# Performance work log

Hardware: AMD Instinct MI355X
Metric: run time of the kernel (lower is better)

Reference implementation:

```python
import jax, jax.numpy as jnp
import numpy as np

L, D, F, H = 4, 1024, 2048, 8
DH = D // H
EPS = 1e-5


def setup_inputs() -> dict:
    key = jax.random.key(0)
    ks = jax.random.split(key, 8)
    B, S = 4, 1024
    sd = 1.0 / np.sqrt(D)
    sf = 1.0 / np.sqrt(F)
    return {
        "X": jax.random.normal(ks[0], (B, S, D), jnp.float32),
        "Wq": jax.random.normal(ks[1], (L, D, D), jnp.float32) * sd,
        "Wk": jax.random.normal(ks[2], (L, D, D), jnp.float32) * sd,
        "Wv": jax.random.normal(ks[3], (L, D, D), jnp.float32) * sd,
        "Wg": jax.random.normal(ks[4], (L, D, D), jnp.float32) * sd,
        "Wo": jax.random.normal(ks[5], (L, D, D), jnp.float32) * sd,
        "W1": jax.random.normal(ks[6], (L, D, F), jnp.float32) * sd,
        "W2": jax.random.normal(ks[7], (L, F, D), jnp.float32) * sf,
        "ln_scale": jnp.ones((D,), jnp.float32),
        "ln_bias": jnp.zeros((D,), jnp.float32),
        "gn_scale": jnp.ones((L, D), jnp.float32),
        "gn_bias": jnp.zeros((L, D), jnp.float32),
    }


def _layer_norm(x, scale, bias):
    mu = x.mean(-1, keepdims=True)
    var = x.var(-1, keepdims=True)
    return (x - mu) * jax.lax.rsqrt(var + EPS) * scale + bias


def _rotate(x, cos, sin):
    # x: (B,S,H,DH); cos/sin: (1,S,1,DH//2); rotary pairs (even, odd)
    x1, x2 = x[..., 0::2], x[..., 1::2]
    r1 = x1 * cos - x2 * sin
    r2 = x1 * sin + x2 * cos
    return jnp.stack([r1, r2], axis=-1).reshape(x.shape)


def _decay_matrix(S):
    # D[h,n,m] = gamma_h^(n-m) for n>=m else 0
    gammas = 1.0 - jnp.exp(jnp.linspace(np.log(1 / 32), np.log(1 / 512), H)).astype(jnp.float32)
    n = jnp.arange(S)
    diff = (n[:, None] - n[None, :]).astype(jnp.float32)
    pw = jnp.exp(jnp.clip(diff, 0.0)[None] * jnp.log(gammas)[:, None, None])
    return jnp.where(diff[None] >= 0, pw, 0.0)  # (H,S,S)


def _retention(x, Wq, Wk, Wv, Wg, Wo, gn_s, gn_b, Dm, cos, sin):
    B, S, _ = x.shape
    Q = (x @ Wq).reshape(B, S, H, DH)
    K = (x @ Wk).reshape(B, S, H, DH)
    V = (x @ Wv).reshape(B, S, H, DH)
    Q = _rotate(Q, cos, sin)
    K = _rotate(K, cos, -sin)  # conjugate phase
    att = jnp.einsum('bnhd,bmhd->bhnm', Q, K) * Dm  # (B,H,S,S)
    Y = jnp.einsum('bhnm,bmhd->bnhd', att, V)
    # group norm: normalize each head's output per token
    mu = Y.mean(-1, keepdims=True)
    var = Y.var(-1, keepdims=True)
    Y = (Y - mu) * jax.lax.rsqrt(var + EPS)
    Y = Y.reshape(B, S, D) * gn_s + gn_b
    G = jax.nn.swish(x @ Wg)
    return (G * Y) @ Wo


def reference(X, Wq, Wk, Wv, Wg, Wo, W1, W2, ln_scale, ln_bias, gn_scale, gn_bias):
    B, S, _ = X.shape
    pos = jnp.arange(S, dtype=jnp.float32)
    inv_freq = 1.0 / (10000.0 ** (jnp.arange(0, DH, 2, dtype=jnp.float32) / DH))
    ang = pos[:, None] * inv_freq[None, :]  # (S, DH//2)
    cos = jnp.cos(ang)[None, :, None, :]
    sin = jnp.sin(ang)[None, :, None, :]
    Dm = _decay_matrix(S)
    for i in range(L):
        Yr = _retention(_layer_norm(X, ln_scale, ln_bias), Wq[i], Wk[i], Wv[i],
                        Wg[i], Wo[i], gn_scale[i], gn_bias[i], Dm, cos, sin) + X
        X = jax.nn.gelu(_layer_norm(Yr, ln_scale, ln_bias) @ W1[i]) @ W2[i] + Yr
    return X
```

## Files before the change

kernel.cpp:

```cpp
#include <hip/hip_runtime.h>
#include <hip/hip_bf16.h>
#include <cmath>

#define LAYERS 4
#define Bb 4
#define Ss 1024
#define Dd 1024
#define Ff 2048
#define Hh 8
#define DHd 128
#define Mm (Bb * Ss)
#define EPSf 1e-5f
#define LDQ 4096

typedef __attribute__((ext_vector_type(8))) short short8v;
typedef __attribute__((ext_vector_type(4))) float f32x4;
typedef __attribute__((ext_vector_type(4))) unsigned int u32x4;

__device__ __forceinline__ float swish_f(float x) { return x / (1.f + expf(-x)); }
__device__ __forceinline__ float gelu_f(float x) {
  return 0.5f * x * (1.f + tanhf(0.7978845608028654f * (x + 0.044715f * x * x * x)));
}
__device__ __forceinline__ unsigned short f2bfu(float f) {
  __hip_bfloat16 h = __float2bfloat16(f);
  return __builtin_bit_cast(unsigned short, h);
}
__device__ __forceinline__ float bfu2f(unsigned short u) {
  unsigned v = ((unsigned)u) << 16;
  return __builtin_bit_cast(float, v);
}
__device__ __forceinline__ void gl_lds16(const void* g, void* l) {
  __builtin_amdgcn_global_load_lds((__attribute__((address_space(1))) void*)g,
                                   (__attribute__((address_space(3))) void*)l, 16, 0, 0);
}
__device__ __forceinline__ f32x4 mfma16(short8v a, short8v b, f32x4 c) {
  return __builtin_amdgcn_mfma_f32_16x16x32_bf16(a, b, c, 0, 0, 0);
}

__global__ __launch_bounds__(256) void ln_bf16_kernel(const float* __restrict__ x,
                                                      short* __restrict__ outb,
                                                      const float* __restrict__ sc,
                                                      const float* __restrict__ bi) {
  const int row = blockIdx.x;
  const int t = threadIdx.x;
  const float4 v = *(const float4*)(x + (size_t)row * Dd + t * 4);
  float s = v.x + v.y + v.z + v.w;
  float s2 = v.x * v.x + v.y * v.y + v.z * v.z + v.w * v.w;
#pragma unroll
  for (int o = 32; o > 0; o >>= 1) { s += __shfl_down(s, o); s2 += __shfl_down(s2, o); }
  __shared__ float ps[4], ps2[4];
  if ((t & 63) == 0) { ps[t >> 6] = s; ps2[t >> 6] = s2; }
  __syncthreads();
  s = ps[0] + ps[1] + ps[2] + ps[3];
  s2 = ps2[0] + ps2[1] + ps2[2] + ps2[3];
  const float mu = s * (1.f / Dd);
  const float var = s2 * (1.f / Dd) - mu * mu;
  const float rstd = rsqrtf(var + EPSf);
  const float4 g = *(const float4*)(sc + t * 4);
  const float4 b = *(const float4*)(bi + t * 4);
  const float o0 = (v.x - mu) * rstd * g.x + b.x;
  const float o1 = (v.y - mu) * rstd * g.y + b.y;
  const float o2 = (v.z - mu) * rstd * g.z + b.z;
  const float o3 = (v.w - mu) * rstd * g.w + b.w;
  unsigned p0 = (unsigned)f2bfu(o0) | ((unsigned)f2bfu(o1) << 16);
  unsigned p1 = (unsigned)f2bfu(o2) | ((unsigned)f2bfu(o3) << 16);
  uint2 pk; pk.x = p0; pk.y = p1;
  *(uint2*)(outb + (size_t)row * Dd + t * 4) = pk;
}

__global__ void rope_table_kernel(float* __restrict__ ct, float* __restrict__ st) {
  const int i = blockIdx.x * 256 + threadIdx.x;
  const int s = i >> 6, f = i & 63;
  const float inv = powf(10000.f, -(float)f / 64.f);
  const float a = (float)s * inv;
  ct[i] = cosf(a);
  st[i] = sinf(a);
}

__global__ void rope_ip_kernel(short* __restrict__ QK, const float* __restrict__ ct,
                               const float* __restrict__ st) {
  const int idx = blockIdx.x * 256 + threadIdx.x;
  const int f = idx & 63;
  const int h = (idx >> 6) & 7;
  const int r = idx >> 9;
  const int s = r & (Ss - 1);
  const float c = ct[(s << 6) + f], sn = st[(s << 6) + f];
  const size_t qo = (size_t)r * LDQ + h * DHd + 2 * f;
  const unsigned qp = *(const unsigned*)(QK + qo);
  const unsigned kp = *(const unsigned*)(QK + qo + 1024);
  const float qx = bfu2f((unsigned short)(qp & 0xffff)), qy = bfu2f((unsigned short)(qp >> 16));
  const float kx = bfu2f((unsigned short)(kp & 0xffff)), ky = bfu2f((unsigned short)(kp >> 16));
  const unsigned qn = (unsigned)f2bfu(qx * c - qy * sn) | ((unsigned)f2bfu(qx * sn + qy * c) << 16);
  const unsigned kn = (unsigned)f2bfu(kx * c + ky * sn) | ((unsigned)f2bfu(-kx * sn + ky * c) << 16);
  *(unsigned*)(QK + qo) = qn;
  *(unsigned*)(QK + qo + 1024) = kn;
}

__global__ __launch_bounds__(256) void wtrans4_kernel(const float* __restrict__ W0,
                                                      const float* __restrict__ W1,
                                                      const float* __restrict__ W2,
                                                      const float* __restrict__ W3,
                                                      short* __restrict__ Wt) {
  __shared__ float tile[32][33];
  const int t = threadIdx.x;
  const int n0 = blockIdx.x * 32, k0 = blockIdx.y * 32;
  const int which = n0 >> 10;
  const float* W = (which == 0) ? W0 : (which == 1) ? W1 : (which == 2) ? W2 : W3;
  const int nl = n0 & 1023;
  const int tc = t & 31, tr8 = t >> 5;
#pragma unroll
  for (int i = 0; i < 4; ++i) {
    const int r = tr8 + i * 8;
    tile[r][tc] = W[(size_t)(k0 + r) * 1024 + nl + tc];
  }
  __syncthreads();
#pragma unroll
  for (int i = 0; i < 4; ++i) {
    const int r = tr8 + i * 8;
    Wt[(size_t)(n0 + r) * 1024 + k0 + tc] = (short)f2bfu(tile[tc][r]);
  }
}

__global__ __launch_bounds__(256) void wtrans1_kernel(const float* __restrict__ W,
                                                      short* __restrict__ Wt, int K, int N) {
  __shared__ float tile[32][33];
  const int t = threadIdx.x;
  const int n0 = blockIdx.x * 32, k0 = blockIdx.y * 32;
  const int tc = t & 31, tr8 = t >> 5;
#pragma unroll
  for (int i = 0; i < 4; ++i) {
    const int r = tr8 + i * 8;
    tile[r][tc] = W[(size_t)(k0 + r) * N + n0 + tc];
  }
  __syncthreads();
#pragma unroll
  for (int i = 0; i < 4; ++i) {
    const int r = tr8 + i * 8;
    Wt[(size_t)(n0 + r) * K + k0 + tc] = (short)f2bfu(tile[tc][r]);
  }
}

__global__ __launch_bounds__(256) void vtrans16_kernel(const short* __restrict__ Vb,
                                                       short* __restrict__ Vt) {
  __shared__ short tile[32][33];
  const int t = threadIdx.x;
  const int s0 = blockIdx.x * 32, d0 = blockIdx.y * 32, bh = blockIdx.z;
  const int bb = bh >> 3, h = bh & 7;
  const int tc = t & 31, tr8 = t >> 5;
#pragma unroll
  for (int i = 0; i < 4; ++i) {
    const int r = tr8 + i * 8;
    tile[r][tc] = Vb[(size_t)(bb * Ss + s0 + r) * LDQ + 2048 + h * DHd + d0 + tc];
  }
  __syncthreads();
#pragma unroll
  for (int i = 0; i < 4; ++i) {
    const int r = tr8 + i * 8;
    Vt[(size_t)(bh * DHd + d0 + r) * Ss + s0 + tc] = tile[tc][r];
  }
}

template <int EPI>
__global__ __launch_bounds__(512, 2) void gemm10(const short* __restrict__ A,
                                                 const short* __restrict__ Bt,
                                                 float* __restrict__ Cf,
                                                 short* __restrict__ Cb,
                                                 const float* __restrict__ Res,
                                                 int N, int K, int ldc) {
  __shared__ __align__(16) short As[2][2][128 * 64];
  __shared__ __align__(16) short Bs[2][2][128 * 64];
  const int t = threadIdx.x;
  const int w = t >> 6, l = t & 63;
  const int lq = l >> 4, lr = l & 15;
  const int wr = w >> 2, wc = w & 3;
  const int bhalf = wc >> 1, brow0 = (wc & 1) * 64;
  const int nwg = gridDim.x * gridDim.y;
  const int bid0 = blockIdx.x + blockIdx.y * gridDim.x;
  const int lgid = (bid0 & 7) * (nwg >> 3) + (bid0 >> 3);
  const int bx = lgid % gridDim.x, by = lgid / gridDim.x;
  const int row0 = by * 256, col0 = bx * 256;
  const int NT = K >> 6;

  f32x4 acc[8][4] = {};
  short8v a[4][2], b[4][2];

  auto stageA = [&](int kt, int hf) {
    const int db = kt & 1;
#pragma unroll
    for (int i = 0; i < 2; ++i) {
      const int c = t + i * 512;
      const int row = c >> 3, slot = c & 7;
      gl_lds16(A + (size_t)(row0 + hf * 128 + row) * K + kt * 64 + ((slot ^ (row & 7)) << 3),
               &As[db][hf][c * 8]);
    }
  };
  auto stageB = [&](int kt, int hf) {
    const int db = kt & 1;
#pragma unroll
    for (int i = 0; i < 2; ++i) {
      const int c = t + i * 512;
      const int row = c >> 3, slot = c & 7;
      gl_lds16(Bt + (size_t)(col0 + hf * 128 + row) * K + kt * 64 + ((slot ^ (row & 7)) << 3),
               &Bs[db][hf][c * 8]);
    }
  };
  auto rdA = [&](int db, int m, int ks) -> short8v {
    const int row = m * 16 + lr;
    return *(const short8v*)&As[db][wr][row * 64 + (((ks << 2) + lq) ^ (row & 7)) * 8];
  };
  auto rdB = [&](int db, int n, int ks) -> short8v {
    const int row = brow0 + n * 16 + lr;
    return *(const short8v*)&Bs[db][bhalf][row * 64 + (((ks << 2) + lq) ^ (row & 7)) * 8];
  };

  stageA(0, 0); stageA(0, 1); stageB(0, 0); stageB(0, 1);
  if (NT > 1) { stageB(1, 0); stageB(1, 1); }
  if (NT > 1) { asm volatile("s_waitcnt vmcnt(4)" ::: "memory"); }
  else        { asm volatile("s_waitcnt vmcnt(0)" ::: "memory"); }
  asm volatile("s_barrier" ::: "memory");

  for (int kt = 0; kt < NT; ++kt) {
    const int db = kt & 1;
#pragma unroll
    for (int m = 0; m < 4; ++m) { a[m][0] = rdA(db, m, 0); a[m][1] = rdA(db, m, 1); }
#pragma unroll
    for (int n = 0; n < 2; ++n) { b[n][0] = rdB(db, n, 0); b[n][1] = rdB(db, n, 1); }
    if (kt + 1 < NT) stageA(kt + 1, 0);
    __builtin_amdgcn_s_setprio(1);
#pragma unroll
    for (int m = 0; m < 4; ++m)
#pragma unroll
      for (int n = 0; n < 2; ++n) {
        acc[m][n] = mfma16(a[m][0], b[n][0], acc[m][n]);
        acc[m][n] = mfma16(a[m][1], b[n][1], acc[m][n]);
      }
    __builtin_amdgcn_s_setprio(0);
    asm volatile("s_barrier" ::: "memory");
#pragma unroll
    for (int n = 2; n < 4; ++n) { b[n][0] = rdB(db, n, 0); b[n][1] = rdB(db, n, 1); }
    if (kt + 1 < NT) stageA(kt + 1, 1);
    __builtin_amdgcn_s_setprio(1);
#pragma unroll
    for (int m = 0; m < 4; ++m)
#pragma unroll
      for (int n = 2; n < 4; ++n) {
        acc[m][n] = mfma16(a[m][0], b[n][0], acc[m][n]);
        acc[m][n] = mfma16(a[m][1], b[n][1], acc[m][n]);
      }
    __builtin_amdgcn_s_setprio(0);
    asm volatile("s_barrier" ::: "memory");
#pragma unroll
    for (int m = 0; m < 4; ++m) { a[m][0] = rdA(db, m + 4, 0); a[m][1] = rdA(db, m + 4, 1); }
    if (kt + 2 < NT) stageB(kt + 2, 0);
    __builtin_amdgcn_s_setprio(1);
#pragma unroll
    for (int m = 0; m < 4; ++m)
#pragma unroll
      for (int n = 0; n < 2; ++n) {
        acc[m + 4][n] = mfma16(a[m][0], b[n][0], acc[m + 4][n]);
        acc[m + 4][n] = mfma16(a[m][1], b[n][1], acc[m + 4][n]);
      }
    __builtin_amdgcn_s_setprio(0);
    asm volatile("s_barrier" ::: "memory");
    if (kt + 2 < NT) stageB(kt + 2, 1);
    __builtin_amdgcn_s_setprio(1);
#pragma unroll
    for (int m = 0; m < 4; ++m)
#pragma unroll
      for (int n = 2; n < 4; ++n) {
        acc[m + 4][n] = mfma16(a[m][0], b[n][0], acc[m + 4][n]);
        acc[m + 4][n] = mfma16(a[m][1], b[n][1], acc[m + 4][n]);
      }
    __builtin_amdgcn_s_setprio(0);
    if (kt + 2 < NT) { asm volatile("s_waitcnt vmcnt(4)" ::: "memory"); }
    else             { asm volatile("s_waitcnt vmcnt(0)" ::: "memory"); }
    asm volatile("s_barrier" ::: "memory");
  }

#pragma unroll
  for (int m = 0; m < 8; ++m) {
#pragma unroll
    for (int n = 0; n < 4; ++n) {
#pragma unroll
      for (int r = 0; r < 4; ++r) {
        const int row = row0 + wr * 128 + m * 16 + lq * 4 + r;
        const int col = col0 + wc * 64 + n * 16 + lr;
        const size_t o = (size_t)row * ldc + col;
        float v = acc[m][n][r];
        if (EPI == 0) Cb[o] = (short)f2bfu(v);
        else if (EPI == 1) Cf[o] = v + Res[o];
        else Cb[o] = (short)f2bfu(gelu_f(v));
      }
    }
  }
}

template <int EPI>
__global__ __launch_bounds__(512) void gemm11(const short* __restrict__ A,
                                              const short* __restrict__ Bt,
                                              float* __restrict__ Cf,
                                              short* __restrict__ Cb,
                                              const float* __restrict__ Res,
                                              int K, int lda, int ldb, int ldc, int nxt) {
  __shared__ __align__(16) short As[3][256 * 64];
  __shared__ __align__(16) short Bs[3][128 * 64];
  const int t = threadIdx.x;
  const int w = t >> 6, l = t & 63;
  const int lq = l >> 4, lr = l & 15;
  const int wr = w >> 2, wc = w & 3;
  const int nwg = gridDim.x;
  const int lgid = (blockIdx.x & 7) * (nwg >> 3) + (blockIdx.x >> 3);
  const int mt = lgid / nxt, nt_ = lgid % nxt;
  const int row0 = mt * 256, col0 = nt_ * 128;
  const int NT = K >> 6;
  f32x4 acc[8][2] = {};
  short8v a[4][2], b[2][2];

  auto stageA = [&](int kt, int hf) {
    const int s = kt % 3;
#pragma unroll
    for (int i = 0; i < 2; ++i) {
      const int c = t + i * 512;
      const int row = c >> 3, slot = c & 7;
      gl_lds16(A + (size_t)(row0 + hf * 128 + row) * lda + kt * 64 + ((slot ^ (row & 7)) << 3),
               &As[s][hf * 8192 + c * 8]);
    }
  };
  auto stageB = [&](int kt) {
    const int s = kt % 3;
#pragma unroll
    for (int i = 0; i < 2; ++i) {
      const int c = t + i * 512;
      const int row = c >> 3, slot = c & 7;
      gl_lds16(Bt + (size_t)(col0 + row) * ldb + kt * 64 + ((slot ^ (row & 7)) << 3),
               &Bs[s][c * 8]);
    }
  };
  auto rdA = [&](int s, int m, int ks) -> short8v {
    const int row = wr * 128 + m * 16 + lr;
    return *(const short8v*)&As[s][row * 64 + (((ks << 2) + lq) ^ (row & 7)) * 8];
  };
  auto rdB = [&](int s, int n, int ks) -> short8v {
    const int row = wc * 32 + n * 16 + lr;
    return *(const short8v*)&Bs[s][row * 64 + (((ks << 2) + lq) ^ (row & 7)) * 8];
  };

  stageA(0, 0); stageA(0, 1); stageB(0);
  stageA(1, 0); stageA(1, 1); stageB(1);
  asm volatile("s_waitcnt vmcnt(6)" ::: "memory");
  asm volatile("s_barrier" ::: "memory");

  for (int kt = 0; kt < NT; ++kt) {
    const int s = kt % 3;
#pragma unroll
    for (int m = 0; m < 4; ++m) { a[m][0] = rdA(s, m, 0); a[m][1] = rdA(s, m, 1); }
#pragma unroll
    for (int n = 0; n < 2; ++n) { b[n][0] = rdB(s, n, 0); b[n][1] = rdB(s, n, 1); }
    if (kt + 2 < NT) stageA(kt + 2, 0);
    __builtin_amdgcn_s_setprio(1);
#pragma unroll
    for (int m = 0; m < 4; ++m)
#pragma unroll
      for (int n = 0; n < 2; ++n) {
        acc[m][n] = mfma16(a[m][0], b[n][0], acc[m][n]);
        acc[m][n] = mfma16(a[m][1], b[n][1], acc[m][n]);
      }
    __builtin_amdgcn_s_setprio(0);
    asm volatile("s_barrier" ::: "memory");
#pragma unroll
    for (int m = 0; m < 4; ++m) { a[m][0] = rdA(s, m + 4, 0); a[m][1] = rdA(s, m + 4, 1); }
    if (kt + 2 < NT) { stageA(kt + 2, 1); stageB(kt + 2); }
    __builtin_amdgcn_s_setprio(1);
#pragma unroll
    for (int m = 0; m < 4; ++m)
#pragma unroll
      for (int n = 0; n < 2; ++n) {
        acc[m + 4][n] = mfma16(a[m][0], b[n][0], acc[m + 4][n]);
        acc[m + 4][n] = mfma16(a[m][1], b[n][1], acc[m + 4][n]);
      }
    __builtin_amdgcn_s_setprio(0);
    if (kt + 2 < NT) { asm volatile("s_waitcnt vmcnt(6)" ::: "memory"); }
    else             { asm volatile("s_waitcnt vmcnt(0)" ::: "memory"); }
    asm volatile("s_barrier" ::: "memory");
  }

#pragma unroll
  for (int m = 0; m < 8; ++m) {
#pragma unroll
    for (int n = 0; n < 2; ++n) {
#pragma unroll
      for (int r = 0; r < 4; ++r) {
        const int row = row0 + wr * 128 + m * 16 + lq * 4 + r;
        const int col = col0 + wc * 32 + n * 16 + lr;
        const size_t o = (size_t)row * ldc + col;
        float v = acc[m][n][r];
        if (EPI == 0) Cb[o] = (short)f2bfu(v);
        else if (EPI == 1) Cf[o] = v + Res[o];
        else Cb[o] = (short)f2bfu(gelu_f(v));
      }
    }
  }
}

template <int EPI>
__global__ __launch_bounds__(512) void gemm12(const short* __restrict__ A,
                                              const short* __restrict__ Bt,
                                              float* __restrict__ Cf,
                                              short* __restrict__ Cb,
                                              const float* __restrict__ Res,
                                              int K, int lda, int ldb, int ldc, int nxt) {
  __shared__ __align__(16) short As[3][128 * 64];
  __shared__ __align__(16) short Bs[3][128 * 64];
  const int t = threadIdx.x;
  const int w = t >> 6, l = t & 63;
  const int lq = l >> 4, lr = l & 15;
  const int wr = w >> 2, wc = w & 3;
  const int nwg = gridDim.x;
  const int lgid = (blockIdx.x & 7) * (nwg >> 3) + (blockIdx.x >> 3);
  const int mt = lgid / nxt, nt_ = lgid % nxt;
  const int row0 = mt * 128, col0 = nt_ * 128;
  const int NT = K >> 6;
  f32x4 acc[4][2] = {};
  short8v a[4][2], b[2][2];

  auto stageA = [&](int kt) {
    const int s = kt % 3;
#pragma unroll
    for (int i = 0; i < 2; ++i) {
      const int c = t + i * 512;
      const int row = c >> 3, slot = c & 7;
      gl_lds16(A + (size_t)(row0 + row) * lda + kt * 64 + ((slot ^ (row & 7)) << 3),
               &As[s][c * 8]);
    }
  };
  auto stageB = [&](int kt) {
    const int s = kt % 3;
#pragma unroll
    for (int i = 0; i < 2; ++i) {
      const int c = t + i * 512;
      const int row = c >> 3, slot = c & 7;
      gl_lds16(Bt + (size_t)(col0 + row) * ldb + kt * 64 + ((slot ^ (row & 7)) << 3),
               &Bs[s][c * 8]);
    }
  };
  auto rdA = [&](int s, int m, int ks) -> short8v {
    const int row = wr * 64 + m * 16 + lr;
    return *(const short8v*)&As[s][row * 64 + (((ks << 2) + lq) ^ (row & 7)) * 8];
  };
  auto rdB = [&](int s, int n, int ks) -> short8v {
    const int row = wc * 32 + n * 16 + lr;
    return *(const short8v*)&Bs[s][row * 64 + (((ks << 2) + lq) ^ (row & 7)) * 8];
  };

  stageA(0); stageB(0);
  stageA(1); stageB(1);
  asm volatile("s_waitcnt vmcnt(4)" ::: "memory");
  asm volatile("s_barrier" ::: "memory");

  for (int kt = 0; kt < NT; ++kt) {
    const int s = kt % 3;
#pragma unroll
    for (int m = 0; m < 4; ++m) { a[m][0] = rdA(s, m, 0); a[m][1] = rdA(s, m, 1); }
#pragma unroll
    for (int n = 0; n < 2; ++n) { b[n][0] = rdB(s, n, 0); b[n][1] = rdB(s, n, 1); }
    if (kt + 2 < NT) stageA(kt + 2);
    __builtin_amdgcn_s_setprio(1);
#pragma unroll
    for (int m = 0; m < 2; ++m)
#pragma unroll
      for (int n = 0; n < 2; ++n) {
        acc[m][n] = mfma16(a[m][0], b[n][0], acc[m][n]);
        acc[m][n] = mfma16(a[m][1], b[n][1], acc[m][n]);
      }
    __builtin_amdgcn_s_setprio(0);
    asm volatile("s_barrier" ::: "memory");
    if (kt + 2 < NT) stageB(kt + 2);
    __builtin_amdgcn_s_setprio(1);
#pragma unroll
    for (int m = 2; m < 4; ++m)
#pragma unroll
      for (int n = 0; n < 2; ++n) {
        acc[m][n] = mfma16(a[m][0], b[n][0], acc[m][n]);
        acc[m][n] = mfma16(a[m][1], b[n][1], acc[m][n]);
      }
    __builtin_amdgcn_s_setprio(0);
    if (kt + 2 < NT) { asm volatile("s_waitcnt vmcnt(4)" ::: "memory"); }
    else             { asm volatile("s_waitcnt vmcnt(0)" ::: "memory"); }
    asm volatile("s_barrier" ::: "memory");
  }

#pragma unroll
  for (int m = 0; m < 4; ++m) {
#pragma unroll
    for (int n = 0; n < 2; ++n) {
#pragma unroll
      for (int r = 0; r < 4; ++r) {
        const int row = row0 + wr * 64 + m * 16 + lq * 4 + r;
        const int col = col0 + wc * 32 + n * 16 + lr;
        const size_t o = (size_t)row * ldc + col;
        float v = acc[m][n][r];
        if (EPI == 0) Cb[o] = (short)f2bfu(v);
        else if (EPI == 1) Cf[o] = v + Res[o];
        else Cb[o] = (short)f2bfu(gelu_f(v));
      }
    }
  }
}

__global__ __launch_bounds__(256) void ret4_kernel(const short* __restrict__ QKb,
                                                   const short* __restrict__ Vt,
                                                   float* __restrict__ Y0,
                                                   float* __restrict__ Y1) {
  __shared__ __align__(16) short Ks[2][64 * 128];
  __shared__ __align__(16) short Vs[2][128 * 64];
  const int t = threadIdx.x, w = t >> 6, l = t & 63;
  const int lq = l >> 4, lr = l & 15;
  const int u = blockIdx.x;
  const int lgid = (u & 7) * 64 + (u >> 3);
  const int half = lgid >> 8;
  const int rest = lgid & 255;
  const int bh = rest >> 3, j = rest & 7;
  const int qb = half ? j : 7 - j;
  const int b = bh >> 3, h = bh & 7;
  const int q0 = qb * 128;
  const float lstep = (logf(1.f / 512.f) - logf(1.f / 32.f)) * (1.f / 7.f);
  const float gamma = 1.f - expf(logf(1.f / 32.f) + (float)h * lstep);
  const float l2g = logf(gamma) * 1.44269504f;
  const short* Qp = QKb;
  const short* Kp = QKb + 1024;

  short8v qf[2][4];
#pragma unroll
  for (int qn = 0; qn < 2; ++qn)
#pragma unroll
    for (int ks = 0; ks < 4; ++ks)
      qf[qn][ks] = *(const short8v*)(Qp + (size_t)(b * Ss + q0 + w * 32 + qn * 16 + lr) * LDQ +
                                     h * DHd + ks * 32 + lq * 8);

  float cmf[4], csr[4];
#pragma unroll
  for (int mf = 0; mf < 4; ++mf) cmf[mf] = exp2f(l2g * (float)(-16 * mf));
#pragma unroll
  for (int r = 0; r < 4; ++r) csr[r] = exp2f(l2g * (float)(63 - 4 * lq - r));

  f32x4 yacc[2][8] = {};
  const int nt = 2 * qb + 2;
  const int sb = ((lq & 1) * 2) * 16 + lr;

  auto stageKV = [&](int m0, int buf) {
#pragma unroll
    for (int i = 0; i < 4; ++i) {
      const int c = (w * 4 + i) * 64 + l;
      const int row = c >> 4, slot = c & 15;
      gl_lds16(Kp + (size_t)(b * Ss + m0 + row) * LDQ + h * DHd + ((slot ^ (row & 7)) * 8),
               &Ks[buf][(w * 4 + i) * 512]);
    }
#pragma unroll
    for (int i = 0; i < 4; ++i) {
      const int c = (w * 4 + i) * 64 + l;
      const int row = c >> 3, slot = c & 7;
      gl_lds16(Vt + (size_t)(bh * DHd + row) * Ss + m0 + ((slot ^ (row & 7)) * 8),
               &Vs[buf][(w * 4 + i) * 512]);
    }
  };

  stageKV(half * 64, 0);
  __syncthreads();
  int cur = 0;
  for (int tt = half; tt < nt; tt += 2) {
    const int m0 = tt * 64;
    if (tt + 2 < nt) stageKV((tt + 2) * 64, cur ^ 1);

    f32x4 st[4][2] = {};
    __builtin_amdgcn_s_setprio(1);
#pragma unroll
    for (int mf = 0; mf < 4; ++mf) {
      const int row = mf * 16 + lr;
#pragma unroll
      for (int ks = 0; ks < 4; ++ks) {
        short8v kf = *(const short8v*)&Ks[cur][row * 128 + (((4 * ks + lq) ^ (row & 7)) * 8)];
        st[mf][0] = mfma16(kf, qf[0][ks], st[mf][0]);
        st[mf][1] = mfma16(kf, qf[1][ks], st[mf][1]);
      }
    }
    __builtin_amdgcn_s_setprio(0);
    float rs[2];
#pragma unroll
    for (int qn = 0; qn < 2; ++qn)
      rs[qn] = exp2f(l2g * (float)(q0 + w * 32 + qn * 16 + lr - m0 - 63));
#pragma unroll
    for (int mf = 0; mf < 4; ++mf)
#pragma unroll
      for (int qn = 0; qn < 2; ++qn)
#pragma unroll
        for (int r = 0; r < 4; ++r) {
          const int qg = q0 + w * 32 + qn * 16 + lr;
          const int kvg = m0 + mf * 16 + lq * 4 + r;
          const float wgt = (qg >= kvg) ? rs[qn] * cmf[mf] * csr[r] : 0.f;
          st[mf][qn][r] *= wgt;
        }
    unsigned pk[4][2][2];
#pragma unroll
    for (int mf = 0; mf < 4; ++mf)
#pragma unroll
      for (int qn = 0; qn < 2; ++qn)
#pragma unroll
        for (int p = 0; p < 2; ++p)
          pk[mf][qn][p] = (unsigned)f2bfu(st[mf][qn][2 * p]) |
                          ((unsigned)f2bfu(st[mf][qn][2 * p + 1]) << 16);
    short8v afr[2][2];
#pragma unroll
    for (int qn = 0; qn < 2; ++qn)
#pragma unroll
      for (int ks2 = 0; ks2 < 2; ++ks2) {
        u32x4 wd;
#pragma unroll
        for (int wj = 0; wj < 4; ++wj) {
          const int src = sb + (wj >> 1) * 16;
          const unsigned v0 = __shfl(pk[2 * ks2 + 0][qn][wj & 1], src);
          const unsigned v1 = __shfl(pk[2 * ks2 + 1][qn][wj & 1], src);
          wd[wj] = (lq >= 2) ? v1 : v0;
        }
        afr[qn][ks2] = __builtin_bit_cast(short8v, wd);
      }
    __builtin_amdgcn_s_setprio(1);
#pragma unroll
    for (int nd = 0; nd < 8; ++nd) {
      const int row = nd * 16 + lr;
#pragma unroll
      for (int ks2 = 0; ks2 < 2; ++ks2) {
        short8v vf = *(const short8v*)&Vs[cur][row * 64 + (((4 * ks2 + lq) ^ (row & 7)) * 8)];
        yacc[0][nd] = mfma16(afr[0][ks2], vf, yacc[0][nd]);
        yacc[1][nd] = mfma16(afr[1][ks2], vf, yacc[1][nd]);
      }
    }
    __builtin_amdgcn_s_setprio(0);
    __syncthreads();
    cur ^= 1;
  }
  float* Y = half ? Y1 : Y0;
#pragma unroll
  for (int qn = 0; qn < 2; ++qn)
#pragma unroll
    for (int r = 0; r < 4; ++r) {
      const int q = q0 + w * 32 + qn * 16 + lq * 4 + r;
#pragma unroll
      for (int nd = 0; nd < 8; ++nd)
        Y[(size_t)(b * Ss + q) * Dd + h * DHd + nd * 16 + lr] = yacc[qn][nd][r];
    }
}

__global__ __launch_bounds__(256) void gate_kernel(const float* __restrict__ Y0,
                                                   const float* __restrict__ Y1,
                                                   const short* __restrict__ Graw,
                                                   short* __restrict__ Gb,
                                                   const float* __restrict__ gs,
                                                   const float* __restrict__ gb) {
  const int lane = threadIdx.x & 63;
  const int rowh = blockIdx.x * 4 + (threadIdx.x >> 6);
  const int h = rowh & 7;
  const int row = rowh >> 3;
  const size_t ybase = (size_t)row * Dd + (size_t)h * DHd + lane * 2;
  float2 a = *(const float2*)(Y0 + ybase);
  const float2 c = *(const float2*)(Y1 + ybase);
  a.x += c.x; a.y += c.y;
  float s = a.x + a.y, s2 = a.x * a.x + a.y * a.y;
#pragma unroll
  for (int o = 32; o > 0; o >>= 1) { s += __shfl_down(s, o); s2 += __shfl_down(s2, o); }
  s = __shfl(s, 0);
  s2 = __shfl(s2, 0);
  const float mu = s * (1.f / DHd);
  const float rstd = rsqrtf(s2 * (1.f / DHd) - mu * mu + EPSf);
  const int d = h * DHd + lane * 2;
  const float2 g = *(const float2*)(gs + d);
  const float2 bbv = *(const float2*)(gb + d);
  const float y0 = (a.x - mu) * rstd * g.x + bbv.x;
  const float y1 = (a.y - mu) * rstd * g.y + bbv.y;
  const unsigned gr = *(const unsigned*)(Graw + (size_t)row * LDQ + 3072 + h * DHd + lane * 2);
  const float gx = bfu2f((unsigned short)(gr & 0xffff));
  const float gy = bfu2f((unsigned short)(gr >> 16));
  const unsigned o01 = (unsigned)f2bfu(swish_f(gx) * y0) |
                       ((unsigned)f2bfu(swish_f(gy) * y1) << 16);
  *(unsigned*)(Gb + ybase) = o01;
}

extern "C" void kernel_launch(void* const* d_in, const int* in_sizes, int n_in,
                              void* d_out, int out_size, void* d_ws, size_t ws_size,
                              hipStream_t stream) {
  const float* X = (const float*)d_in[0];
  const float* Wq = (const float*)d_in[1];
  const float* Wk = (const float*)d_in[2];
  const float* Wv = (const float*)d_in[3];
  const float* Wg = (const float*)d_in[4];
  const float* Wo = (const float*)d_in[5];
  const float* W1 = (const float*)d_in[6];
  const float* W2 = (const float*)d_in[7];
  const float* lns = (const float*)d_in[8];
  const float* lnb = (const float*)d_in[9];
  const float* gns = (const float*)d_in[10];
  const float* gnb = (const float*)d_in[11];
  float* out = (float*)d_out;

  char* W = (char*)d_ws;
  const size_t MB = 1u << 20;
  float* Abuf  = (float*)(W);
  short* Xnb   = (short*)(W + 16 * MB);
  short* QKVGb = (short*)(W + 24 * MB);
  float* Y0    = (float*)(W + 56 * MB);
  float* Y1    = (float*)(W + 72 * MB);
  short* Vtb   = (short*)(W + 88 * MB);
  short* Gb    = (short*)(W + 96 * MB);
  short* Wqkvgt= (short*)(W + 104 * MB);
  short* Wot   = (short*)(W + 112 * MB);
  short* W1t   = (short*)(W + 114 * MB);
  short* W2t   = (short*)(W + 118 * MB);
  float* ct    = (float*)(W + 122 * MB);
  float* st    = ct + Ss * 64;
  short* Hb = QKVGb;

  hipMemcpyAsync(Abuf, X, (size_t)Mm * Dd * sizeof(float), hipMemcpyDeviceToDevice, stream);
  rope_table_kernel<<<(Ss * 64) / 256, 256, 0, stream>>>(ct, st);

  for (int l = 0; l < LAYERS; ++l) {
    const size_t DD = (size_t)Dd * Dd;
    wtrans4_kernel<<<dim3(128, 32), 256, 0, stream>>>(Wq + l * DD, Wk + l * DD, Wv + l * DD,
                                                      Wg + l * DD, Wqkvgt);
    wtrans1_kernel<<<dim3(32, 32), 256, 0, stream>>>(Wo + l * DD, Wot, Dd, Dd);
    wtrans1_kernel<<<dim3(64, 32), 256, 0, stream>>>(W1 + (size_t)l * Dd * Ff, W1t, Dd, Ff);
    wtrans1_kernel<<<dim3(32, 64), 256, 0, stream>>>(W2 + (size_t)l * Ff * Dd, W2t, Ff, Dd);

    ln_bf16_kernel<<<Mm, 256, 0, stream>>>(Abuf, Xnb, lns, lnb);
    gemm10<0><<<dim3(16, 16), 512, 0, stream>>>(Xnb, Wqkvgt, nullptr, QKVGb,
                                                nullptr, 4096, Dd, LDQ);
    rope_ip_kernel<<<(Bb * Ss * Hh * 64) / 256, 256, 0, stream>>>(QKVGb, ct, st);
    vtrans16_kernel<<<dim3(Ss / 32, DHd / 32, Bb * Hh), 256, 0, stream>>>(QKVGb, Vtb);
    ret4_kernel<<<512, 256, 0, stream>>>(QKVGb, Vtb, Y0, Y1);
    gate_kernel<<<(Mm * Hh) / 4, 256, 0, stream>>>(Y0, Y1, QKVGb, Gb,
                                                   gns + (size_t)l * Dd, gnb + (size_t)l * Dd);
    gemm12<1><<<256, 512, 0, stream>>>(Gb, Wot, Abuf, nullptr, Abuf,
                                       Dd, Dd, Dd, Dd, 8);
    ln_bf16_kernel<<<Mm, 256, 0, stream>>>(Abuf, Xnb, lns, lnb);
    gemm11<2><<<256, 512, 0, stream>>>(Xnb, W1t, nullptr, Hb, nullptr,
                                       Dd, Dd, Dd, Ff, 16);
    float* dst = (l == LAYERS - 1) ? out : Abuf;
    gemm12<1><<<256, 512, 0, stream>>>(Hb, W2t, dst, nullptr, Abuf,
                                       Ff, Ff, Ff, Dd, 8);
  }
}
```

Baseline: 767.4 us.

## Merge weight transposes and rope/V-transpose launches; prefetch A two tiles ahead

```diff
diff --git a/kernel.cpp b/kernel.cpp
--- a/kernel.cpp
+++ b/kernel.cpp
@@ -77,91 +77,95 @@
   st[i] = sinf(a);
 }
 
-__global__ void rope_ip_kernel(short* __restrict__ QK, const float* __restrict__ ct,
-                               const float* __restrict__ st) {
-  const int idx = blockIdx.x * 256 + threadIdx.x;
-  const int f = idx & 63;
-  const int h = (idx >> 6) & 7;
-  const int r = idx >> 9;
-  const int s = r & (Ss - 1);
-  const float c = ct[(s << 6) + f], sn = st[(s << 6) + f];
-  const size_t qo = (size_t)r * LDQ + h * DHd + 2 * f;
-  const unsigned qp = *(const unsigned*)(QK + qo);
-  const unsigned kp = *(const unsigned*)(QK + qo + 1024);
-  const float qx = bfu2f((unsigned short)(qp & 0xffff)), qy = bfu2f((unsigned short)(qp >> 16));
-  const float kx = bfu2f((unsigned short)(kp & 0xffff)), ky = bfu2f((unsigned short)(kp >> 16));
-  const unsigned qn = (unsigned)f2bfu(qx * c - qy * sn) | ((unsigned)f2bfu(qx * sn + qy * c) << 16);
-  const unsigned kn = (unsigned)f2bfu(kx * c + ky * sn) | ((unsigned)f2bfu(-kx * sn + ky * c) << 16);
-  *(unsigned*)(QK + qo) = qn;
-  *(unsigned*)(QK + qo + 1024) = kn;
-}
-
-__global__ __launch_bounds__(256) void wtrans4_kernel(const float* __restrict__ W0,
-                                                      const float* __restrict__ W1,
-                                                      const float* __restrict__ W2,
-                                                      const float* __restrict__ W3,
-                                                      short* __restrict__ Wt) {
+__global__ __launch_bounds__(256) void wtrans_all_kernel(
+    const float* __restrict__ Wq, const float* __restrict__ Wk,
+    const float* __restrict__ Wv, const float* __restrict__ Wg,
+    const float* __restrict__ Wo, const float* __restrict__ W1,
+    const float* __restrict__ W2,
+    short* __restrict__ Wqkvgt, short* __restrict__ Wot,
+    short* __restrict__ W1t, short* __restrict__ W2t) {
   __shared__ float tile[32][33];
   const int t = threadIdx.x;
-  const int n0 = blockIdx.x * 32, k0 = blockIdx.y * 32;
-  const int which = n0 >> 10;
-  const float* W = (which == 0) ? W0 : (which == 1) ? W1 : (which == 2) ? W2 : W3;
-  const int nl = n0 & 1023;
   const int tc = t & 31, tr8 = t >> 5;
+  const int blk = blockIdx.x;
+  const float* src; short* dst; int K, N, n0, k0, nl;
+  if (blk < 4096) {
+    const int bx = blk & 127, ky = blk >> 7;
+    n0 = bx * 32; k0 = ky * 32;
+    const int which = n0 >> 10;
+    src = (which == 0) ? Wq : (which == 1) ? Wk : (which == 2) ? Wv : Wg;
+    nl = n0 & 1023; N = 1024; K = 1024; dst = Wqkvgt;
+  } else if (blk < 5120) {
+    const int b2 = blk - 4096;
+    n0 = (b2 & 31) * 32; k0 = (b2 >> 5) * 32; nl = n0;
+    src = Wo; N = 1024; K = 1024; dst = Wot;
+  } else if (blk < 7168) {
+    const int b2 = blk - 5120;
+    n0 = (b2 & 63) * 32; k0 = (b2 >> 6) * 32; nl = n0;
+    src = W1; N = 2048; K = 1024; dst = W1t;
+  } else {
+    const int b2 = blk - 7168;
+    n0 = (b2 & 31) * 32; k0 = (b2 >> 5) * 32; nl = n0;
+    src = W2; N = 1024; K = 2048; dst = W2t;
+  }
 #pragma unroll
   for (int i = 0; i < 4; ++i) {
     const int r = tr8 + i * 8;
-    tile[r][tc] = W[(size_t)(k0 + r) * 1024 + nl + tc];
+    tile[r][tc] = src[(size_t)(k0 + r) * N + nl + tc];
   }
   __syncthreads();
 #pragma unroll
   for (int i = 0; i < 4; ++i) {
     const int r = tr8 + i * 8;
-    Wt[(size_t)(n0 + r) * 1024 + k0 + tc] = (short)f2bfu(tile[tc][r]);
-  }
-}
-
-__global__ __launch_bounds__(256) void wtrans1_kernel(const float* __restrict__ W,
-                                                      short* __restrict__ Wt, int K, int N) {
-  __shared__ float tile[32][33];
-  const int t = threadIdx.x;
-  const int n0 = blockIdx.x * 32, k0 = blockIdx.y * 32;
-  const int tc = t & 31, tr8 = t >> 5;
-#pragma unroll
-  for (int i = 0; i < 4; ++i) {
-    const int r = tr8 + i * 8;
-    tile[r][tc] = W[(size_t)(k0 + r) * N + n0 + tc];
-  }
-  __syncthreads();
-#pragma unroll
-  for (int i = 0; i < 4; ++i) {
-    const int r = tr8 + i * 8;
-    Wt[(size_t)(n0 + r) * K + k0 + tc] = (short)f2bfu(tile[tc][r]);
-  }
-}
-
-__global__ __launch_bounds__(256) void vtrans16_kernel(const short* __restrict__ Vb,
-                                                       short* __restrict__ Vt) {
+    dst[(size_t)(n0 + r) * K + k0 + tc] = (short)f2bfu(tile[tc][r]);
+  }
+}
+
+__global__ __launch_bounds__(256) void rvt_kernel(short* __restrict__ QKVGb,
+                                                  short* __restrict__ Vt,
+                                                  const float* __restrict__ ct,
+                                                  const float* __restrict__ st) {
   __shared__ short tile[32][33];
-  const int t = threadIdx.x;
-  const int s0 = blockIdx.x * 32, d0 = blockIdx.y * 32, bh = blockIdx.z;
-  const int bb = bh >> 3, h = bh & 7;
-  const int tc = t & 31, tr8 = t >> 5;
-#pragma unroll
-  for (int i = 0; i < 4; ++i) {
-    const int r = tr8 + i * 8;
-    tile[r][tc] = Vb[(size_t)(bb * Ss + s0 + r) * LDQ + 2048 + h * DHd + d0 + tc];
-  }
-  __syncthreads();
-#pragma unroll
-  for (int i = 0; i < 4; ++i) {
-    const int r = tr8 + i * 8;
-    Vt[(size_t)(bh * DHd + d0 + r) * Ss + s0 + tc] = tile[tc][r];
+  const int blk = blockIdx.x, t = threadIdx.x;
+  if (blk < 8192) {
+    const int idx = blk * 256 + t;
+    const int f = idx & 63;
+    const int h = (idx >> 6) & 7;
+    const int r = idx >> 9;
+    const int s = r & (Ss - 1);
+    const float c = ct[(s << 6) + f], sn = st[(s << 6) + f];
+    const size_t qo = (size_t)r * LDQ + h * DHd + 2 * f;
+    const unsigned qp = *(const unsigned*)(QKVGb + qo);
+    const unsigned kp = *(const unsigned*)(QKVGb + qo + 1024);
+    const float qx = bfu2f((unsigned short)(qp & 0xffff)), qy = bfu2f((unsigned short)(qp >> 16));
+    const float kx = bfu2f((unsigned short)(kp & 0xffff)), ky = bfu2f((unsigned short)(kp >> 16));
+    const unsigned qn = (unsigned)f2bfu(qx * c - qy * sn) |
+                        ((unsigned)f2bfu(qx * sn + qy * c) << 16);
+    const unsigned kn = (unsigned)f2bfu(kx * c + ky * sn) |
+                        ((unsigned)f2bfu(-kx * sn + ky * c) << 16);
+    *(unsigned*)(QKVGb + qo) = qn;
+    *(unsigned*)(QKVGb + qo + 1024) = kn;
+  } else {
+    const int vb = blk - 8192;
+    const int s0 = (vb & 31) * 32, d0 = ((vb >> 5) & 3) * 32, bh = vb >> 7;
+    const int bb = bh >> 3, h = bh & 7;
+    const int tc = t & 31, tr8 = t >> 5;
+#pragma unroll
+    for (int i = 0; i < 4; ++i) {
+      const int r = tr8 + i * 8;
+      tile[r][tc] = QKVGb[(size_t)(bb * Ss + s0 + r) * LDQ + 2048 + h * DHd + d0 + tc];
+    }
+    __syncthreads();
+#pragma unroll
+    for (int i = 0; i < 4; ++i) {
+      const int r = tr8 + i * 8;
+      Vt[(size_t)(bh * DHd + d0 + r) * Ss + s0 + tc] = tile[tc][r];
+    }
   }
 }
 
 template <int EPI>
-__global__ __launch_bounds__(512, 2) void gemm10(const short* __restrict__ A,
+__global__ __launch_bounds__(512, 2) void gemm13(const short* __restrict__ A,
                                                  const short* __restrict__ Bt,
                                                  float* __restrict__ Cf,
                                                  short* __restrict__ Cb,
@@ -214,8 +218,8 @@
   };
 
   stageA(0, 0); stageA(0, 1); stageB(0, 0); stageB(0, 1);
-  if (NT > 1) { stageB(1, 0); stageB(1, 1); }
-  if (NT > 1) { asm volatile("s_waitcnt vmcnt(4)" ::: "memory"); }
+  if (NT > 1) { stageA(1, 0); stageA(1, 1); stageB(1, 0); stageB(1, 1); }
+  if (NT > 1) { asm volatile("s_waitcnt vmcnt(8)" ::: "memory"); }
   else        { asm volatile("s_waitcnt vmcnt(0)" ::: "memory"); }
   asm volatile("s_barrier" ::: "memory");
 
@@ -225,7 +229,6 @@
     for (int m = 0; m < 4; ++m) { a[m][0] = rdA(db, m, 0); a[m][1] = rdA(db, m, 1); }
 #pragma unroll
     for (int n = 0; n < 2; ++n) { b[n][0] = rdB(db, n, 0); b[n][1] = rdB(db, n, 1); }
-    if (kt + 1 < NT) stageA(kt + 1, 0);
     __builtin_amdgcn_s_setprio(1);
 #pragma unroll
     for (int m = 0; m < 4; ++m)
@@ -238,7 +241,6 @@
     asm volatile("s_barrier" ::: "memory");
 #pragma unroll
     for (int n = 2; n < 4; ++n) { b[n][0] = rdB(db, n, 0); b[n][1] = rdB(db, n, 1); }
-    if (kt + 1 < NT) stageA(kt + 1, 1);
     __builtin_amdgcn_s_setprio(1);
 #pragma unroll
     for (int m = 0; m < 4; ++m)
@@ -251,7 +253,7 @@
     asm volatile("s_barrier" ::: "memory");
 #pragma unroll
     for (int m = 0; m < 4; ++m) { a[m][0] = rdA(db, m + 4, 0); a[m][1] = rdA(db, m + 4, 1); }
-    if (kt + 2 < NT) stageB(kt + 2, 0);
+    if (kt + 2 < NT) { stageB(kt + 2, 0); stageB(kt + 2, 1); }
     __builtin_amdgcn_s_setprio(1);
 #pragma unroll
     for (int m = 0; m < 4; ++m)
@@ -262,7 +264,7 @@
       }
     __builtin_amdgcn_s_setprio(0);
     asm volatile("s_barrier" ::: "memory");
-    if (kt + 2 < NT) stageB(kt + 2, 1);
+    if (kt + 2 < NT) { stageA(kt + 2, 0); stageA(kt + 2, 1); }
     __builtin_amdgcn_s_setprio(1);
 #pragma unroll
     for (int m = 0; m < 4; ++m)
@@ -272,7 +274,7 @@
         acc[m + 4][n] = mfma16(a[m][1], b[n][1], acc[m + 4][n]);
       }
     __builtin_amdgcn_s_setprio(0);
-    if (kt + 2 < NT) { asm volatile("s_waitcnt vmcnt(4)" ::: "memory"); }
+    if (kt + 2 < NT) { asm volatile("s_waitcnt vmcnt(8)" ::: "memory"); }
     else             { asm volatile("s_waitcnt vmcnt(0)" ::: "memory"); }
     asm volatile("s_barrier" ::: "memory");
   }
@@ -723,17 +725,15 @@
 
   for (int l = 0; l < LAYERS; ++l) {
     const size_t DD = (size_t)Dd * Dd;
-    wtrans4_kernel<<<dim3(128, 32), 256, 0, stream>>>(Wq + l * DD, Wk + l * DD, Wv + l * DD,
-                                                      Wg + l * DD, Wqkvgt);
-    wtrans1_kernel<<<dim3(32, 32), 256, 0, stream>>>(Wo + l * DD, Wot, Dd, Dd);
-    wtrans1_kernel<<<dim3(64, 32), 256, 0, stream>>>(W1 + (size_t)l * Dd * Ff, W1t, Dd, Ff);
-    wtrans1_kernel<<<dim3(32, 64), 256, 0, stream>>>(W2 + (size_t)l * Ff * Dd, W2t, Ff, Dd);
-
+    wtrans_all_kernel<<<9216, 256, 0, stream>>>(Wq + l * DD, Wk + l * DD, Wv + l * DD,
+                                                Wg + l * DD, Wo + l * DD,
+                                                W1 + (size_t)l * Dd * Ff,
+                                                W2 + (size_t)l * Ff * Dd,
+                                                Wqkvgt, Wot, W1t, W2t);
     ln_bf16_kernel<<<Mm, 256, 0, stream>>>(Abuf, Xnb, lns, lnb);
-    gemm10<0><<<dim3(16, 16), 512, 0, stream>>>(Xnb, Wqkvgt, nullptr, QKVGb,
+    gemm13<0><<<dim3(16, 16), 512, 0, stream>>>(Xnb, Wqkvgt, nullptr, QKVGb,
                                                 nullptr, 4096, Dd, LDQ);
-    rope_ip_kernel<<<(Bb * Ss * Hh * 64) / 256, 256, 0, stream>>>(QKVGb, ct, st);
-    vtrans16_kernel<<<dim3(Ss / 32, DHd / 32, Bb * Hh), 256, 0, stream>>>(QKVGb, Vtb);
+    rvt_kernel<<<12288, 256, 0, stream>>>(QKVGb, Vtb, ct, st);
     ret4_kernel<<<512, 256, 0, stream>>>(QKVGb, Vtb, Y0, Y1);
     gate_kernel<<<(Mm * Hh) / 4, 256, 0, stream>>>(Y0, Y1, QKVGb, Gb,
                                                    gns + (size_t)l * Dd, gnb + (size_t)l * Dd);
```

Result: no change. 757.4 us (-1.3%).
